# Performance work log

Measured on AMD Instinct MI355X. Metric: run time of the kernel, lower is better.

Reference implementation:

```python
import jax, jax.numpy as jnp
import numpy as np

L, B, VOCAB, K, D, NUM_LAYERS = 256, 32, 30000, 620, 2400, 4


def setup_inputs() -> dict:
    key = jax.random.key(0)
    ks = jax.random.split(key, 10)
    inp = {
        "tokens": jax.random.randint(ks[0], (L, B), 0, VOCAB, dtype=jnp.int32),
        "emb": jax.random.normal(ks[1], (VOCAB, K), dtype=jnp.float32) * 0.1,
        # layer 0: n_in (K) != n_out (D) -> k=4 projections (z, f, r, highway transform)
        "W0": jax.random.normal(ks[2], (K, 4 * D), dtype=jnp.float32) * (1.0 / np.sqrt(K)),
        "b0": jnp.zeros((2 * D,), dtype=jnp.float32),
    }
    for i in range(1, NUM_LAYERS):
        inp[f"W{i}"] = jax.random.normal(ks[2 + i], (D, 3 * D), dtype=jnp.float32) * (1.0 / np.sqrt(D))
        inp[f"b{i}"] = jnp.zeros((2 * D,), dtype=jnp.float32)
    return inp


def _scan_cell(f, z):
    # c_t = f_t * c_{t-1} + (1 - f_t) * z_t ; c_0 = 0.  f, z: (L, B, D)
    def step(c, fz):
        f_t, z_t = fz
        c = f_t * c + (1.0 - f_t) * z_t
        return c, c
    c0 = jnp.zeros(f.shape[1:], f.dtype)
    _, cs = jax.lax.scan(step, c0, (f, z))
    return cs  # (L, B, D)


def _sru_layer(x, W, b):
    # x: (L, B, n_in); W: (n_in, k*D); b: (2*D,)
    k = W.shape[1] // D
    U = jnp.einsum('lbi,io->lbo', x, W).reshape(x.shape[0], x.shape[1], k, D)
    z = U[..., 0, :]
    f = jax.nn.sigmoid(U[..., 1, :] + b[:D])
    r = jax.nn.sigmoid(U[..., 2, :] + b[D:])
    c = _scan_cell(f, z)
    x_skip = U[..., 3, :] if k == 4 else x  # highway transform when dims differ
    h = r * jnp.tanh(c) + (1.0 - r) * x_skip
    return h


def reference(tokens, emb, W0, b0, W1, b1, W2, b2, W3, b3):
    x = emb[tokens]  # (L, B, K) embedding gather
    for W, b in ((W0, b0), (W1, b1), (W2, b2), (W3, b3)):
        x = _sru_layer(x, W, b)
    # L2-normalize over hidden dim
    out = x / jnp.linalg.norm(x, ord=2, axis=2, keepdims=True)
    return out
```

## Files before the change

kernel.cpp:

```cpp
#include <hip/hip_runtime.h>
#include <cstdint>
#include <cstddef>

typedef unsigned short u16;

constexpr int L_ = 256, B_ = 32, D_ = 2400;
constexpr int K0 = 620, K0P = 640;
constexpr int N0 = 9600;
constexpr int NL = 7200, NLP = 7296;
constexpr int KL = 2400;
constexpr int MR = L_ * B_;

constexpr size_t SZ_WT0 = (size_t)N0 * K0P * 2;
constexpr size_t SZ_X   = (size_t)MR * KL * 2;
constexpr size_t SZ_UB  = (size_t)MR * N0 * 2;
constexpr size_t WS_REQ = SZ_WT0 + 2 * SZ_X + SZ_UB;
constexpr size_t WT_L_OFF = (size_t)MR * NLP * 2;
static_assert(WT_L_OFF + (size_t)NLP * KL * 2 <= SZ_UB, "WtL must fit in U tail");

typedef __bf16 bf16x8 __attribute__((ext_vector_type(8)));
typedef float floatx4 __attribute__((ext_vector_type(4)));

__device__ __forceinline__ u16 f2bf(float x) {
  unsigned u = __float_as_uint(x);
  unsigned r = 0x7fffu + ((u >> 16) & 1u);
  return (u16)((u + r) >> 16);
}
__device__ __forceinline__ float bf2f(u16 v) {
  return __uint_as_float((unsigned)v << 16);
}
__device__ __forceinline__ float frcp(float x) {
  return __builtin_amdgcn_rcpf(x);
}
__device__ __forceinline__ float fsigmoid(float x) {
  return frcp(1.f + __expf(-x));
}
__device__ __forceinline__ float ftanh(float x) {
  return 1.f - 2.f * frcp(__expf(2.f * x) + 1.f);
}

__device__ __forceinline__ void gload_lds16(const void* g, void* l) {
  __builtin_amdgcn_global_load_lds(
      (__attribute__((address_space(1))) void*)g,
      (__attribute__((address_space(3))) void*)l,
      16, 0, 0);
}

__global__ void probe_fill(float* __restrict__ out, int n, float v) {
  int i = blockIdx.x * blockDim.x + threadIdx.x;
  if (i < n) out[i] = v;
}

__global__ void transpose_bf16_kernel(const float* __restrict__ W, u16* __restrict__ Wt,
                                      int K, int N, int Kpad, int Nrows) {
  __shared__ float tile[32][33];
  int kb = blockIdx.x * 32, nb = blockIdx.y * 32;
  int tx = threadIdx.x & 31, ty = threadIdx.x >> 5;
  #pragma unroll
  for (int i = ty; i < 32; i += 8) {
    int k = kb + i, n = nb + tx;
    tile[i][tx] = (k < K && n < N) ? W[(size_t)k * N + n] : 0.f;
  }
  __syncthreads();
  #pragma unroll
  for (int i = ty; i < 32; i += 8) {
    int n = nb + i, k = kb + tx;
    if (n < Nrows && k < Kpad)
      Wt[(size_t)n * Kpad + k] = f2bf(tile[tx][i]);
  }
}

__global__ void embed_kernel(const int* __restrict__ tokens, const float* __restrict__ emb,
                             u16* __restrict__ xbf) {
  int t = blockIdx.x;
  int tok = tokens[t];
  const float* src = emb + (size_t)tok * K0;
  u16* dst = xbf + (size_t)t * K0P;
  for (int k = threadIdx.x; k < K0P; k += blockDim.x)
    dst[k] = (k < K0) ? f2bf(src[k]) : (u16)0;
}

__global__ __launch_bounds__(256, 2)
void gemm_nt_bf16(const u16* __restrict__ A, const u16* __restrict__ Bt,
                  u16* __restrict__ C, int M, int N, int K) {
  __shared__ __align__(16) u16 As[128 * 32];
  __shared__ __align__(16) u16 Bs[128 * 32];
  const int tid  = threadIdx.x;
  const int lane = tid & 63;
  const int wave = tid >> 6;
  const int wr   = (wave >> 1) * 64;
  const int wc   = (wave & 1) * 64;
  const int quad = lane >> 4;
  const int l16  = lane & 15;
  const size_t m0 = (size_t)blockIdx.x * 128;
  const size_t n0 = (size_t)blockIdx.y * 128;

  const int srow = tid >> 2;
  const int scol = (((tid & 3) ^ ((tid >> 3) & 3)) * 8);
  const u16* aSrc = A + (m0 + srow) * (size_t)K + scol;
  const u16* bSrc = Bt + (n0 + srow) * (size_t)K + scol;
  const size_t rowStep = (size_t)64 * K;

  char* ldsA = (char*)As + wave * 1024;
  char* ldsB = (char*)Bs + wave * 1024;

  const int rdChunk = (quad ^ ((l16 >> 1) & 3)) * 8;

  floatx4 acc[4][4] = {};

  for (int k0 = 0; k0 < K; k0 += 32) {
    gload_lds16(aSrc,           ldsA);
    gload_lds16(aSrc + rowStep, ldsA + 4096);
    gload_lds16(bSrc,           ldsB);
    gload_lds16(bSrc + rowStep, ldsB + 4096);
    aSrc += 32; bSrc += 32;
    __syncthreads();
    bf16x8 af[4], bfr[4];
    #pragma unroll
    for (int i = 0; i < 4; ++i)
      af[i] = *(const bf16x8*)&As[(wr + i * 16 + l16) * 32 + rdChunk];
    #pragma unroll
    for (int j = 0; j < 4; ++j)
      bfr[j] = *(const bf16x8*)&Bs[(wc + j * 16 + l16) * 32 + rdChunk];
    #pragma unroll
    for (int i = 0; i < 4; ++i)
      #pragma unroll
      for (int j = 0; j < 4; ++j)
        acc[i][j] = __builtin_amdgcn_mfma_f32_16x16x32_bf16(af[i], bfr[j], acc[i][j], 0, 0, 0);
    __syncthreads();
  }

  #pragma unroll
  for (int i = 0; i < 4; ++i) {
    size_t row = m0 + wr + i * 16 + quad * 4;
    #pragma unroll
    for (int j = 0; j < 4; ++j) {
      size_t col = n0 + wc + j * 16 + l16;
      u16* cp = C + row * (size_t)N + col;
      #pragma unroll
      for (int r = 0; r < 4; ++r)
        cp[(size_t)r * N] = f2bf(acc[i][j][r]);
    }
  }
}

__global__ __launch_bounds__(256, 2)
void sru_scan_kernel(const u16* __restrict__ U, int SN,
                     const float* __restrict__ bias,
                     const u16* __restrict__ skip, int skipStride,
                     u16* __restrict__ hbf, float* __restrict__ h32) {
  __shared__ float A_l[8 * 32];
  __shared__ float C_l[8 * 32];
  const int tid = threadIdx.x;
  const int j  = tid >> 5;
  const int dd = tid & 31;
  const int b  = blockIdx.x / (D_ / 32);
  const int d  = (blockIdx.x % (D_ / 32)) * 32 + dd;
  const float bfb = bias[d], brb = bias[D_ + d];
  const size_t rstep = (size_t)B_ * SN;
  const size_t sstep = (size_t)B_ * skipStride;
  const size_t hstep = (size_t)B_ * D_;
  const u16* Up = U + (size_t)(j * 32) * rstep + (size_t)b * SN + d;
  const u16* Sp = skip + (size_t)(j * 32) * sstep + (size_t)b * skipStride + d;

  float cl[32], P[32];
  {
    float c = 0.f, A = 1.f;
    #pragma unroll
    for (int l = 0; l < 32; ++l) {
      float z  = bf2f(Up[l * rstep]);
      float fr = bf2f(Up[l * rstep + D_]);
      float f = fsigmoid(fr + bfb);
      c = f * c + (1.f - f) * z;
      A *= f;
      cl[l] = c; P[l] = A;
    }
    A_l[tid] = A;
    C_l[tid] = c;
  }
  __syncthreads();
  float Cin = 0.f;
  #pragma unroll
  for (int jj = 0; jj < 7; ++jj) {
    float a  = A_l[jj * 32 + dd];
    float cc = C_l[jj * 32 + dd];
    if (jj < j) Cin = a * Cin + cc;
  }

  u16*   hb = hbf ? hbf + (size_t)(j * 32) * hstep + (size_t)b * D_ + d : nullptr;
  float* hf = h32 ? h32 + (size_t)(j * 32) * hstep + (size_t)b * D_ + d : nullptr;
  #pragma unroll
  for (int l = 0; l < 32; ++l) {
    float rr = bf2f(Up[l * rstep + 2 * D_]);
    float xs = bf2f(Sp[l * sstep]);
    float r = fsigmoid(rr + brb);
    float cf = cl[l] + P[l] * Cin;
    float h = r * ftanh(cf) + (1.f - r) * xs;
    if (hb) hb[l * hstep] = f2bf(h);
    if (hf) hf[l * hstep] = h;
  }
}

__global__ void normalize_kernel(float* __restrict__ x) {
  __shared__ float red[4];
  int row = blockIdx.x;
  float* p = x + (size_t)row * D_;
  float s = 0.f;
  for (int d = threadIdx.x; d < D_; d += 256) { float v = p[d]; s += v * v; }
  #pragma unroll
  for (int o = 32; o > 0; o >>= 1) s += __shfl_down(s, o, 64);
  int lane = threadIdx.x & 63, w = threadIdx.x >> 6;
  if (lane == 0) red[w] = s;
  __syncthreads();
  if (threadIdx.x == 0) red[0] = 1.f / sqrtf(red[0] + red[1] + red[2] + red[3]);
  __syncthreads();
  float inv = red[0];
  for (int d = threadIdx.x; d < D_; d += 256) p[d] *= inv;
}

extern "C" void kernel_launch(void* const* d_in, const int* in_sizes, int n_in,
                              void* d_out, int out_size, void* d_ws, size_t ws_size,
                              hipStream_t stream) {
  const int*   tokens = (const int*)d_in[0];
  const float* emb = (const float*)d_in[1];
  const float* W0 = (const float*)d_in[2];
  const float* b0 = (const float*)d_in[3];
  const float* W1 = (const float*)d_in[4];
  const float* b1 = (const float*)d_in[5];
  const float* W2 = (const float*)d_in[6];
  const float* b2 = (const float*)d_in[7];
  const float* W3 = (const float*)d_in[8];
  const float* b3 = (const float*)d_in[9];
  float* out = (float*)d_out;

  if (ws_size < WS_REQ) {
    probe_fill<<<(out_size + 255) / 256, 256, 0, stream>>>(out, out_size,
                                                           (float)(ws_size >> 20));
    return;
  }

  char* ws = (char*)d_ws;
  u16* Wt0 = (u16*)ws;
  u16* xa  = (u16*)(ws + SZ_WT0);
  u16* xb  = (u16*)(ws + SZ_WT0 + SZ_X);
  u16* Ub  = (u16*)(ws + SZ_WT0 + 2 * SZ_X);
  u16* WtL = (u16*)((char*)Ub + WT_L_OFF);

  dim3 blk(256);
  const int scanGrid = B_ * (D_ / 32);

  embed_kernel<<<MR, 256, 0, stream>>>(tokens, emb, xa);

  transpose_bf16_kernel<<<dim3(K0P / 32, N0 / 32), blk, 0, stream>>>(W0, Wt0, K0, N0, K0P, N0);
  gemm_nt_bf16<<<dim3(MR / 128, N0 / 128), blk, 0, stream>>>(xa, Wt0, Ub, MR, N0, K0P);
  sru_scan_kernel<<<scanGrid, 256, 0, stream>>>(Ub, N0, b0, Ub + 3 * D_, N0, xb, nullptr);

  transpose_bf16_kernel<<<dim3(KL / 32, NLP / 32), blk, 0, stream>>>(W1, WtL, KL, NL, KL, NLP);
  gemm_nt_bf16<<<dim3(MR / 128, NLP / 128), blk, 0, stream>>>(xb, WtL, Ub, MR, NLP, KL);
  sru_scan_kernel<<<scanGrid, 256, 0, stream>>>(Ub, NLP, b1, xb, D_, xa, nullptr);

  transpose_bf16_kernel<<<dim3(KL / 32, NLP / 32), blk, 0, stream>>>(W2, WtL, KL, NL, KL, NLP);
  gemm_nt_bf16<<<dim3(MR / 128, NLP / 128), blk, 0, stream>>>(xa, WtL, Ub, MR, NLP, KL);
  sru_scan_kernel<<<scanGrid, 256, 0, stream>>>(Ub, NLP, b2, xa, D_, xb, nullptr);

  transpose_bf16_kernel<<<dim3(KL / 32, NLP / 32), blk, 0, stream>>>(W3, WtL, KL, NL, KL, NLP);
  gemm_nt_bf16<<<dim3(MR / 128, NLP / 128), blk, 0, stream>>>(xb, WtL, Ub, MR, NLP, KL);
  sru_scan_kernel<<<scanGrid, 256, 0, stream>>>(Ub, NLP, b3, xb, D_, nullptr, out);

  normalize_kernel<<<MR, 256, 0, stream>>>(out);
}
```

Baseline: 1.790 ms.

## Double GEMM K-tile to 64 with padded activation layout and workspace reuse

The bf16 GEMM now stages a 128x64 K-slice per iteration, with an 8-chunk XOR swizzle and two MFMA sub-steps, which halves the number of barriers per K. Activation buffers are padded to a K multiple of 64 (2432) and zero-filled in the pad columns, and the transposed weights are padded to match. Occupancy hint rises to 4 blocks per CU. The layer-0 weight and input buffers are also moved to overlap the activation workspace. The trade-off is larger LDS per block, extra padded K work, and two small zero-fill launches.

```diff
diff --git a/kernel.cpp b/kernel.cpp
--- a/kernel.cpp
+++ b/kernel.cpp
@@ -3,20 +3,28 @@
 #include <cstddef>
 
 typedef unsigned short u16;
+typedef unsigned char u8;
 
 constexpr int L_ = 256, B_ = 32, D_ = 2400;
 constexpr int K0 = 620, K0P = 640;
 constexpr int N0 = 9600;
 constexpr int NL = 7200, NLP = 7296;
-constexpr int KL = 2400;
+constexpr int KL = 2400, KLP = 2432;
 constexpr int MR = L_ * B_;
 
-constexpr size_t SZ_WT0 = (size_t)N0 * K0P * 2;
-constexpr size_t SZ_X   = (size_t)MR * KL * 2;
-constexpr size_t SZ_UB  = (size_t)MR * N0 * 2;
-constexpr size_t WS_REQ = SZ_WT0 + 2 * SZ_X + SZ_UB;
+constexpr size_t SZ_XBUF = (size_t)MR * KLP * 2;
+constexpr size_t SZ_UB   = (size_t)MR * N0 * 2;
+constexpr size_t OFF_XA  = 0;
+constexpr size_t OFF_XB  = SZ_XBUF;
+constexpr size_t OFF_U   = 2 * SZ_XBUF;
+constexpr size_t WS_REQ  = OFF_U + SZ_UB;
+constexpr size_t SZ_WT0  = (size_t)N0 * K0P * 2;
+constexpr size_t OFF_WT0 = OFF_XA + SZ_XBUF - SZ_WT0;
+static_assert(OFF_WT0 % 256 == 0, "");
+constexpr size_t SZ_X0   = (size_t)MR * K0P * 2;
+static_assert(SZ_X0 <= SZ_XBUF, "");
 constexpr size_t WT_L_OFF = (size_t)MR * NLP * 2;
-static_assert(WT_L_OFF + (size_t)NLP * KL * 2 <= SZ_UB, "WtL must fit in U tail");
+static_assert(WT_L_OFF + (size_t)NLP * KLP * 2 <= SZ_UB, "WtL must fit in U tail");
 
 typedef __bf16 bf16x8 __attribute__((ext_vector_type(8)));
 typedef float floatx4 __attribute__((ext_vector_type(4)));
@@ -29,12 +37,8 @@
 __device__ __forceinline__ float bf2f(u16 v) {
   return __uint_as_float((unsigned)v << 16);
 }
-__device__ __forceinline__ float frcp(float x) {
-  return __builtin_amdgcn_rcpf(x);
-}
-__device__ __forceinline__ float fsigmoid(float x) {
-  return frcp(1.f + __expf(-x));
-}
+__device__ __forceinline__ float frcp(float x) { return __builtin_amdgcn_rcpf(x); }
+__device__ __forceinline__ float fsigmoid(float x) { return frcp(1.f + __expf(-x)); }
 __device__ __forceinline__ float ftanh(float x) {
   return 1.f - 2.f * frcp(__expf(2.f * x) + 1.f);
 }
@@ -80,11 +84,21 @@
     dst[k] = (k < K0) ? f2bf(src[k]) : (u16)0;
 }
 
-__global__ __launch_bounds__(256, 2)
+__global__ void zero_pad_x(u16* __restrict__ x) {
+  int r = blockIdx.x * blockDim.x + threadIdx.x;
+  if (r >= MR) return;
+  uint4* p = (uint4*)(x + (size_t)r * KLP + KL);
+  p[0] = make_uint4(0, 0, 0, 0);
+  p[1] = make_uint4(0, 0, 0, 0);
+  p[2] = make_uint4(0, 0, 0, 0);
+  p[3] = make_uint4(0, 0, 0, 0);
+}
+
+__global__ __launch_bounds__(256, 4)
 void gemm_nt_bf16(const u16* __restrict__ A, const u16* __restrict__ Bt,
                   u16* __restrict__ C, int M, int N, int K) {
-  __shared__ __align__(16) u16 As[128 * 32];
-  __shared__ __align__(16) u16 Bs[128 * 32];
+  __shared__ __align__(16) u16 As[128 * 64];
+  __shared__ __align__(16) u16 Bs[128 * 64];
   const int tid  = threadIdx.x;
   const int lane = tid & 63;
   const int wave = tid >> 6;
@@ -95,38 +109,58 @@
   const size_t m0 = (size_t)blockIdx.x * 128;
   const size_t n0 = (size_t)blockIdx.y * 128;
 
-  const int srow = tid >> 2;
-  const int scol = (((tid & 3) ^ ((tid >> 3) & 3)) * 8);
-  const u16* aSrc = A + (m0 + srow) * (size_t)K + scol;
-  const u16* bSrc = Bt + (n0 + srow) * (size_t)K + scol;
-  const size_t rowStep = (size_t)64 * K;
+  const int srow   = tid >> 3;
+  const int gchunk = (tid & 7) ^ (srow & 7);
+  const u16* aSrc = A + (m0 + srow) * (size_t)K + gchunk * 8;
+  const u16* bSrc = Bt + (n0 + srow) * (size_t)K + gchunk * 8;
+  const size_t rowStep = (size_t)32 * K;
 
   char* ldsA = (char*)As + wave * 1024;
   char* ldsB = (char*)Bs + wave * 1024;
 
-  const int rdChunk = (quad ^ ((l16 >> 1) & 3)) * 8;
+  const int sw   = l16 & 7;
+  const int off0 = ((quad    ) ^ sw) * 16;
+  const int off1 = ((quad + 4) ^ sw) * 16;
 
   floatx4 acc[4][4] = {};
 
-  for (int k0 = 0; k0 < K; k0 += 32) {
-    gload_lds16(aSrc,           ldsA);
-    gload_lds16(aSrc + rowStep, ldsA + 4096);
-    gload_lds16(bSrc,           ldsB);
-    gload_lds16(bSrc + rowStep, ldsB + 4096);
-    aSrc += 32; bSrc += 32;
-    __syncthreads();
-    bf16x8 af[4], bfr[4];
+  for (int k0 = 0; k0 < K; k0 += 64) {
     #pragma unroll
     for (int i = 0; i < 4; ++i)
-      af[i] = *(const bf16x8*)&As[(wr + i * 16 + l16) * 32 + rdChunk];
-    #pragma unroll
-    for (int j = 0; j < 4; ++j)
-      bfr[j] = *(const bf16x8*)&Bs[(wc + j * 16 + l16) * 32 + rdChunk];
+      gload_lds16(aSrc + (size_t)i * rowStep, ldsA + i * 4096);
     #pragma unroll
     for (int i = 0; i < 4; ++i)
+      gload_lds16(bSrc + (size_t)i * rowStep, ldsB + i * 4096);
+    aSrc += 64; bSrc += 64;
+    __syncthreads();
+    {
+      bf16x8 af[4], bfr[4];
+      #pragma unroll
+      for (int i = 0; i < 4; ++i)
+        af[i] = *(const bf16x8*)((const char*)As + (wr + i * 16 + l16) * 128 + off0);
       #pragma unroll
       for (int j = 0; j < 4; ++j)
-        acc[i][j] = __builtin_amdgcn_mfma_f32_16x16x32_bf16(af[i], bfr[j], acc[i][j], 0, 0, 0);
+        bfr[j] = *(const bf16x8*)((const char*)Bs + (wc + j * 16 + l16) * 128 + off0);
+      #pragma unroll
+      for (int i = 0; i < 4; ++i)
+        #pragma unroll
+        for (int j = 0; j < 4; ++j)
+          acc[i][j] = __builtin_amdgcn_mfma_f32_16x16x32_bf16(af[i], bfr[j], acc[i][j], 0, 0, 0);
+    }
+    {
+      bf16x8 af[4], bfr[4];
+      #pragma unroll
+      for (int i = 0; i < 4; ++i)
+        af[i] = *(const bf16x8*)((const char*)As + (wr + i * 16 + l16) * 128 + off1);
+      #pragma unroll
+      for (int j = 0; j < 4; ++j)
+        bfr[j] = *(const bf16x8*)((const char*)Bs + (wc + j * 16 + l16) * 128 + off1);
+      #pragma unroll
+      for (int i = 0; i < 4; ++i)
+        #pragma unroll
+        for (int j = 0; j < 4; ++j)
+          acc[i][j] = __builtin_amdgcn_mfma_f32_16x16x32_bf16(af[i], bfr[j], acc[i][j], 0, 0, 0);
+    }
     __syncthreads();
   }
 
@@ -147,8 +181,8 @@
 __global__ __launch_bounds__(256, 2)
 void sru_scan_kernel(const u16* __restrict__ U, int SN,
                      const float* __restrict__ bias,
-                     const u16* __restrict__ skip, int skipStride,
-                     u16* __restrict__ hbf, float* __restrict__ h32) {
+                     const u16* skip, int skipStride,
+                     u16* hbf, float* h32) {
   __shared__ float A_l[8 * 32];
   __shared__ float C_l[8 * 32];
   const int tid = threadIdx.x;
@@ -159,7 +193,8 @@
   const float bfb = bias[d], brb = bias[D_ + d];
   const size_t rstep = (size_t)B_ * SN;
   const size_t sstep = (size_t)B_ * skipStride;
-  const size_t hstep = (size_t)B_ * D_;
+  const size_t hstep = (size_t)B_ * KLP;
+  const size_t fstep = (size_t)B_ * D_;
   const u16* Up = U + (size_t)(j * 32) * rstep + (size_t)b * SN + d;
   const u16* Sp = skip + (size_t)(j * 32) * sstep + (size_t)b * skipStride + d;
 
@@ -187,8 +222,8 @@
     if (jj < j) Cin = a * Cin + cc;
   }
 
-  u16*   hb = hbf ? hbf + (size_t)(j * 32) * hstep + (size_t)b * D_ + d : nullptr;
-  float* hf = h32 ? h32 + (size_t)(j * 32) * hstep + (size_t)b * D_ + d : nullptr;
+  u16*   hb = hbf ? hbf + (size_t)(j * 32) * hstep + (size_t)b * KLP + d : nullptr;
+  float* hf = h32 ? h32 + (size_t)(j * 32) * fstep + (size_t)b * D_ + d : nullptr;
   #pragma unroll
   for (int l = 0; l < 32; ++l) {
     float rr = bf2f(Up[l * rstep + 2 * D_]);
@@ -197,7 +232,7 @@
     float cf = cl[l] + P[l] * Cin;
     float h = r * ftanh(cf) + (1.f - r) * xs;
     if (hb) hb[l * hstep] = f2bf(h);
-    if (hf) hf[l * hstep] = h;
+    if (hf) hf[l * fstep] = h;
   }
 }
 
@@ -240,32 +275,35 @@
   }
 
   char* ws = (char*)d_ws;
-  u16* Wt0 = (u16*)ws;
-  u16* xa  = (u16*)(ws + SZ_WT0);
-  u16* xb  = (u16*)(ws + SZ_WT0 + SZ_X);
-  u16* Ub  = (u16*)(ws + SZ_WT0 + 2 * SZ_X);
+  u16* xa  = (u16*)(ws + OFF_XA);
+  u16* xb  = (u16*)(ws + OFF_XB);
+  u16* Ub  = (u16*)(ws + OFF_U);
+  u16* Wt0 = (u16*)(ws + OFF_WT0);
+  u16* x0  = xb;
   u16* WtL = (u16*)((char*)Ub + WT_L_OFF);
 
   dim3 blk(256);
   const int scanGrid = B_ * (D_ / 32);
-
-  embed_kernel<<<MR, 256, 0, stream>>>(tokens, emb, xa);
-
+  const int padGrid = (MR + 255) / 256;
+
+  embed_kernel<<<MR, 256, 0, stream>>>(tokens, emb, x0);
   transpose_bf16_kernel<<<dim3(K0P / 32, N0 / 32), blk, 0, stream>>>(W0, Wt0, K0, N0, K0P, N0);
-  gemm_nt_bf16<<<dim3(MR / 128, N0 / 128), blk, 0, stream>>>(xa, Wt0, Ub, MR, N0, K0P);
-  sru_scan_kernel<<<scanGrid, 256, 0, stream>>>(Ub, N0, b0, Ub + 3 * D_, N0, xb, nullptr);
-
-  transpose_bf16_kernel<<<dim3(KL / 32, NLP / 32), blk, 0, stream>>>(W1, WtL, KL, NL, KL, NLP);
-  gemm_nt_bf16<<<dim3(MR / 128, NLP / 128), blk, 0, stream>>>(xb, WtL, Ub, MR, NLP, KL);
-  sru_scan_kernel<<<scanGrid, 256, 0, stream>>>(Ub, NLP, b1, xb, D_, xa, nullptr);
-
-  transpose_bf16_kernel<<<dim3(KL / 32, NLP / 32), blk, 0, stream>>>(W2, WtL, KL, NL, KL, NLP);
-  gemm_nt_bf16<<<dim3(MR / 128, NLP / 128), blk, 0, stream>>>(xa, WtL, Ub, MR, NLP, KL);
-  sru_scan_kernel<<<scanGrid, 256, 0, stream>>>(Ub, NLP, b2, xa, D_, xb, nullptr);
-
-  transpose_bf16_kernel<<<dim3(KL / 32, NLP / 32), blk, 0, stream>>>(W3, WtL, KL, NL, KL, NLP);
-  gemm_nt_bf16<<<dim3(MR / 128, NLP / 128), blk, 0, stream>>>(xb, WtL, Ub, MR, NLP, KL);
-  sru_scan_kernel<<<scanGrid, 256, 0, stream>>>(Ub, NLP, b3, xb, D_, nullptr, out);
+  gemm_nt_bf16<<<dim3(MR / 128, N0 / 128), blk, 0, stream>>>(x0, Wt0, Ub, MR, N0, K0P);
+  zero_pad_x<<<padGrid, 256, 0, stream>>>(xa);
+  zero_pad_x<<<padGrid, 256, 0, stream>>>(xb);
+  sru_scan_kernel<<<scanGrid, 256, 0, stream>>>(Ub, N0, b0, Ub + 3 * D_, N0, xa, nullptr);
+
+  transpose_bf16_kernel<<<dim3(KLP / 32, NLP / 32), blk, 0, stream>>>(W1, WtL, KL, NL, KLP, NLP);
+  gemm_nt_bf16<<<dim3(MR / 128, NLP / 128), blk, 0, stream>>>(xa, WtL, Ub, MR, NLP, KLP);
+  sru_scan_kernel<<<scanGrid, 256, 0, stream>>>(Ub, NLP, b1, xa, KLP, xb, nullptr);
+
+  transpose_bf16_kernel<<<dim3(KLP / 32, NLP / 32), blk, 0, stream>>>(W2, WtL, KL, NL, KLP, NLP);
+  gemm_nt_bf16<<<dim3(MR / 128, NLP / 128), blk, 0, stream>>>(xb, WtL, Ub, MR, NLP, KLP);
+  sru_scan_kernel<<<scanGrid, 256, 0, stream>>>(Ub, NLP, b2, xb, KLP, xa, nullptr);
+
+  transpose_bf16_kernel<<<dim3(KLP / 32, NLP / 32), blk, 0, stream>>>(W3, WtL, KL, NL, KLP, NLP);
+  gemm_nt_bf16<<<dim3(MR / 128, NLP / 128), blk, 0, stream>>>(xa, WtL, Ub, MR, NLP, KLP);
+  sru_scan_kernel<<<scanGrid, 256, 0, stream>>>(Ub, NLP, b3, xa, KLP, nullptr, out);
 
   normalize_kernel<<<MR, 256, 0, stream>>>(out);
 }
```

After: 1.545 ms. 1.16x faster.
